# Optimization experiments

Measured on AMD Instinct MI355X. Metric: run time of the kernel, lower is better.

Reference implementation:

```python
import jax, jax.numpy as jnp
import numpy as np

H, W = 8, 64
HK, WK = 7, 11
N = H * W            # 512 tokens
C = 512              # embed_dim
HEADS = 8
HD = C // HEADS      # 64
SCALE = HD ** -0.5
B = 32


def build_local_mask():
    # Faithful port of the build() mask construction.
    m = np.ones([N, H + HK - 1, W + WK - 1], dtype=np.int32)
    for h in range(H):
        for w in range(W):
            m[h * W + w, h:h + HK, w:w + WK] = 0
    m = m[:, HK // 2:H + HK // 2, WK // 2:W + WK // 2].reshape(-1, N).astype(bool)
    mask = np.where(m, -1e30, 0.0).astype(np.float32)
    return jnp.asarray(mask.reshape(1, 1, N, N))


def setup_inputs() -> dict:
    key = jax.random.key(0)
    k1, k2, k3, k4 = jax.random.split(key, 4)
    return {
        "x": jax.random.normal(k1, (B, N, C), dtype=jnp.float32),
        "w_qkv": jax.random.normal(k2, (C, 3 * C), dtype=jnp.float32) * (C ** -0.5),
        "w_proj": jax.random.normal(k3, (C, C), dtype=jnp.float32) * (C ** -0.5),
        "b_proj": jax.random.normal(k4, (C,), dtype=jnp.float32) * 0.01,
        "mask": build_local_mask(),
    }


def reference(x, w_qkv, w_proj, b_proj, mask):
    b = x.shape[0]
    qkv = x @ w_qkv                                   # [B, N, 3C]
    qkv = qkv.reshape(b, N, 3, HEADS, HD)
    qkv = jnp.transpose(qkv, (2, 0, 3, 1, 4))          # [3, B, heads, N, hd]
    q, k, v = qkv[0], qkv[1], qkv[2]
    attn = jnp.einsum("bhnd,bhmd->bhnm", q * SCALE, k) + mask  # [B, heads, N, N]
    attn = jax.nn.softmax(attn, axis=-1)
    out = jnp.einsum("bhnm,bhmd->bhnd", attn, v)       # [B, heads, N, hd]
    out = jnp.transpose(out, (0, 2, 1, 3)).reshape(b, N, C)
    return out @ w_proj + b_proj
```

## Files before the change

### kernel.cpp

```cpp
#include <hip/hip_runtime.h>
#include <hip/hip_bf16.h>

typedef __attribute__((ext_vector_type(8))) __bf16 bf16x8;
typedef __attribute__((ext_vector_type(4))) float f32x4;

__device__ __forceinline__ unsigned short f2bf(float f) {
    unsigned int u = __float_as_uint(f);
    unsigned int r = u + 0x7FFFu + ((u >> 16) & 1u);
    return (unsigned short)(r >> 16);
}

__device__ __forceinline__ void async_copy16(const unsigned short* g, unsigned short* l) {
    __builtin_amdgcn_global_load_lds(
        (__attribute__((address_space(1))) void*)(g),
        (__attribute__((address_space(3))) void*)(l), 16, 0, 0);
}

__global__ __launch_bounds__(256) void cvt_f32_bf16(const float4* __restrict__ in,
                                                    uint4* __restrict__ out, int n8) {
    int i = blockIdx.x * blockDim.x + threadIdx.x;
    if (i >= n8) return;
    float4 a = in[2 * i], b = in[2 * i + 1];
    union { unsigned short s[8]; uint4 v; } r;
    r.s[0] = f2bf(a.x); r.s[1] = f2bf(a.y); r.s[2] = f2bf(a.z); r.s[3] = f2bf(a.w);
    r.s[4] = f2bf(b.x); r.s[5] = f2bf(b.y); r.s[6] = f2bf(b.z); r.s[7] = f2bf(b.w);
    out[i] = r.v;
}

__global__ __launch_bounds__(256) void transpose_cvt(const float* __restrict__ in,
                                                     unsigned short* __restrict__ out,
                                                     int R, int C) {
    __shared__ float tile[32][33];
    int c0 = blockIdx.x * 32, r0 = blockIdx.y * 32;
    int tx = threadIdx.x, ty = threadIdx.y;
    #pragma unroll
    for (int i = 0; i < 32; i += 8)
        tile[ty + i][tx] = in[(size_t)(r0 + ty + i) * C + c0 + tx];
    __syncthreads();
    #pragma unroll
    for (int i = 0; i < 32; i += 8)
        out[(size_t)(c0 + ty + i) * R + r0 + tx] = f2bf(tile[tx][ty + i]);
}

__device__ __forceinline__ void gemm_core_128(const unsigned short* __restrict__ A,
                                              const unsigned short* __restrict__ Bt,
                                              int K, int m0, int n0, f32x4 acc[4][4]) {
    __shared__ unsigned short As[128 * 64];
    __shared__ unsigned short Bs[128 * 64];
    const int lane = threadIdx.x & 63;
    const int wv   = threadIdx.x >> 6;
    const int wm = (wv >> 1) * 64, wn = (wv & 1) * 64;
    const int l15 = lane & 15, l16 = lane >> 4;

    f32x4 zz = {0.f, 0.f, 0.f, 0.f};
    #pragma unroll
    for (int i = 0; i < 4; ++i)
        #pragma unroll
        for (int j = 0; j < 4; ++j) acc[i][j] = zz;

    for (int k0 = 0; k0 < K; k0 += 64) {
        if (k0) __syncthreads();
        #pragma unroll
        for (int c = 0; c < 4; ++c) {
            int flat16 = c * 256 + (int)threadIdx.x;
            int r  = flat16 >> 3;
            int kk = (flat16 & 7) * 8;
            async_copy16(A  + (size_t)(m0 + r) * K + k0 + kk, As + flat16 * 8);
            async_copy16(Bt + (size_t)(n0 + r) * K + k0 + kk, Bs + flat16 * 8);
        }
        __syncthreads();
        #pragma unroll
        for (int kk = 0; kk < 64; kk += 32) {
            bf16x8 a[4], b[4];
            #pragma unroll
            for (int i = 0; i < 4; ++i)
                a[i] = *(const bf16x8*)(const void*)(As + (wm + i * 16 + l15) * 64 + kk + l16 * 8);
            #pragma unroll
            for (int i = 0; i < 4; ++i)
                b[i] = *(const bf16x8*)(const void*)(Bs + (wn + i * 16 + l15) * 64 + kk + l16 * 8);
            #pragma unroll
            for (int i = 0; i < 4; ++i)
                #pragma unroll
                for (int j = 0; j < 4; ++j)
                    acc[i][j] = __builtin_amdgcn_mfma_f32_16x16x32_bf16(a[i], b[j], acc[i][j], 0, 0, 0);
        }
    }
}

__global__ __launch_bounds__(256) void gemm_qkv(const unsigned short* __restrict__ xb,
                                                const unsigned short* __restrict__ wT,
                                                unsigned short* __restrict__ Qb,
                                                unsigned short* __restrict__ Kb,
                                                unsigned short* __restrict__ Vb) {
    f32x4 acc[4][4];
    int m0 = blockIdx.y * 128, n0 = blockIdx.x * 128;
    gemm_core_128(xb, wT, 512, m0, n0, acc);
    const int lane = threadIdx.x & 63, wv = threadIdx.x >> 6;
    const int wm = (wv >> 1) * 64, wn = (wv & 1) * 64;
    const int l15 = lane & 15, l16 = lane >> 4;
    #pragma unroll
    for (int j = 0; j < 4; ++j) {
        int col = n0 + wn + j * 16 + l15;
        int t = col >> 9;
        int within = col & 511;
        int h = within >> 6, d = within & 63;
        unsigned short* dst = (t == 0) ? Qb : (t == 1) ? Kb : Vb;
        float scl = (t == 0) ? 0.125f : 1.0f;
        #pragma unroll
        for (int i = 0; i < 4; ++i)
            #pragma unroll
            for (int e = 0; e < 4; ++e) {
                int row = m0 + wm + i * 16 + (l16 << 2) + e;
                int b = row >> 9, n = row & 511;
                dst[(((size_t)b * 8 + h) * 512 + n) * 64 + d] = f2bf(acc[i][j][e] * scl);
            }
    }
}

__global__ __launch_bounds__(256, 4) void attn_kernel(const unsigned short* __restrict__ Qb,
                                                      const unsigned short* __restrict__ Kb,
                                                      const unsigned short* __restrict__ Vb,
                                                      unsigned short* __restrict__ Ob) {
    __shared__ unsigned short Ks[64 * 72];
    __shared__ unsigned short Vt[64 * 72];
    __shared__ unsigned short Ps[4 * 32 * 72];

    const int bh = blockIdx.x >> 2;
    const int qt = blockIdx.x & 3;
    const int tid = threadIdx.x;
    const int lane = tid & 63;
    const int wv = tid >> 6;
    const int l15 = lane & 15, l16 = lane >> 4;
    const int b = bh >> 3, h = bh & 7;

    const unsigned short* Qp = Qb + (size_t)bh * 512 * 64;
    const unsigned short* Kp = Kb + (size_t)bh * 512 * 64;
    const unsigned short* Vp = Vb + (size_t)bh * 512 * 64;
    unsigned short* Pw = Ps + wv * 32 * 72;

    const int qrow0 = qt * 128 + wv * 32;
    const int qh = qrow0 >> 6;
    const int wq0 = qrow0 & 63;
    const int dead_g = wq0 ? 0 : 3;

    unsigned int wbits = 0;
    {
        int qw[2] = { wq0 + l15, wq0 + 16 + l15 };
        #pragma unroll
        for (int qf = 0; qf < 2; ++qf)
            #pragma unroll
            for (int g = 0; g < 4; ++g)
                #pragma unroll
                for (int j = 0; j < 4; ++j) {
                    int kw = g * 16 + (l16 << 2) + j;
                    int dw = qw[qf] - kw; dw = dw < 0 ? -dw : dw;
                    wbits |= (dw <= 5 ? 1u : 0u) << (qf * 16 + g * 4 + j);
                }
    }

    bf16x8 bQ[2][2];
    #pragma unroll
    for (int qf = 0; qf < 2; ++qf)
        #pragma unroll
        for (int kf = 0; kf < 2; ++kf)
            bQ[qf][kf] = *(const bf16x8*)(const void*)(Qp + (size_t)(qrow0 + qf * 16 + l15) * 64 + kf * 32 + l16 * 8);

    f32x4 o[2][4];
    f32x4 zz = {0.f, 0.f, 0.f, 0.f};
    float mrow[2] = {-INFINITY, -INFINITY}, lrow[2] = {0.f, 0.f};
    #pragma unroll
    for (int qf = 0; qf < 2; ++qf)
        #pragma unroll
        for (int df = 0; df < 4; ++df) o[qf][df] = zz;

    for (int kh = 0; kh < 8; ++kh) {
        int dlo = kh - 2 * qt;
        if (dlo < -3 || dlo > 4) continue;
        __syncthreads();
        #pragma unroll
        for (int c = 0; c < 2; ++c) {
            int flat16 = c * 256 + tid;
            int key = flat16 >> 3, dk = (flat16 & 7) * 8;
            *(uint4*)(void*)(Ks + key * 72 + dk) = *(const uint4*)(const void*)(Kp + ((size_t)(kh * 64 + key) * 64 + dk));
        }
        #pragma unroll
        for (int c = 0; c < 2; ++c) {
            int flat16 = c * 256 + tid;
            int key = flat16 & 63, d8 = flat16 >> 6;
            union { uint4 v; unsigned short s[8]; } t;
            t.v = *(const uint4*)(const void*)(Vp + ((size_t)(kh * 64 + key) * 64 + d8 * 8));
            #pragma unroll
            for (int e = 0; e < 8; ++e) Vt[(d8 * 8 + e) * 72 + key] = t.s[e];
        }
        __syncthreads();

        int adq = qh - kh; adq = adq < 0 ? -adq : adq;
        if (adq > 3) continue;

        f32x4 s[2][4];
        #pragma unroll
        for (int qf = 0; qf < 2; ++qf)
            #pragma unroll
            for (int g = 0; g < 4; ++g) s[qf][g] = zz;
        #pragma unroll
        for (int g = 0; g < 4; ++g) {
            if (g == dead_g) continue;
            bf16x8 aK0 = *(const bf16x8*)(const void*)(Ks + (g * 16 + l15) * 72 + 0  + l16 * 8);
            bf16x8 aK1 = *(const bf16x8*)(const void*)(Ks + (g * 16 + l15) * 72 + 32 + l16 * 8);
            #pragma unroll
            for (int qf = 0; qf < 2; ++qf) {
                s[qf][g] = __builtin_amdgcn_mfma_f32_16x16x32_bf16(aK0, bQ[qf][0], s[qf][g], 0, 0, 0);
                s[qf][g] = __builtin_amdgcn_mfma_f32_16x16x32_bf16(aK1, bQ[qf][1], s[qf][g], 0, 0, 0);
            }
        }

        float tmax[2] = {-1e30f, -1e30f};
        #pragma unroll
        for (int qf = 0; qf < 2; ++qf) {
            #pragma unroll
            for (int g = 0; g < 4; ++g) {
                if (g == dead_g) continue;
                #pragma unroll
                for (int j = 0; j < 4; ++j) {
                    float v = ((wbits >> (qf * 16 + g * 4 + j)) & 1u) ? s[qf][g][j] : -1e30f;
                    s[qf][g][j] = v;
                    tmax[qf] = fmaxf(tmax[qf], v);
                }
            }
            float t = tmax[qf];
            t = fmaxf(t, __shfl_xor(t, 16));
            t = fmaxf(t, __shfl_xor(t, 32));
            tmax[qf] = t;
        }

        #pragma unroll
        for (int qf = 0; qf < 2; ++qf) {
            float mnew = fmaxf(mrow[qf], tmax[qf]);
            float fs = __expf(mrow[qf] - mnew);
            mrow[qf] = mnew;
            lrow[qf] *= fs;
            #pragma unroll
            for (int j = 0; j < 4; ++j) {
                float fso = __shfl(fs, (l16 << 2) + j);
                #pragma unroll
                for (int df = 0; df < 4; ++df) o[qf][df][j] *= fso;
            }
        }

        #pragma unroll
        for (int qf = 0; qf < 2; ++qf) {
            float lsum = 0.f;
            #pragma unroll
            for (int g = 0; g < 4; ++g) {
                unsigned int lo, hi;
                if (g == dead_g) {
                    lo = 0u; hi = 0u;
                } else {
                    float e0 = __expf(s[qf][g][0] - mrow[qf]);
                    float e1 = __expf(s[qf][g][1] - mrow[qf]);
                    float e2 = __expf(s[qf][g][2] - mrow[qf]);
                    float e3 = __expf(s[qf][g][3] - mrow[qf]);
                    lsum += (e0 + e1) + (e2 + e3);
                    asm("v_cvt_pk_bf16_f32 %0, %1, %2" : "=v"(lo) : "v"(e0), "v"(e1));
                    asm("v_cvt_pk_bf16_f32 %0, %1, %2" : "=v"(hi) : "v"(e2), "v"(e3));
                }
                uint2 w; w.x = lo; w.y = hi;
                *(uint2*)(void*)(Pw + (qf * 16 + l15) * 72 + g * 16 + (l16 << 2)) = w;
            }
            float t = lsum;
            t += __shfl_xor(t, 16);
            t += __shfl_xor(t, 32);
            lrow[qf] += t;
        }
        asm volatile("" ::: "memory");

        #pragma unroll
        for (int kf = 0; kf < 2; ++kf) {
            bf16x8 aP0 = *(const bf16x8*)(const void*)(Pw + (0 * 16 + l15) * 72 + kf * 32 + l16 * 8);
            bf16x8 aP1 = *(const bf16x8*)(const void*)(Pw + (1 * 16 + l15) * 72 + kf * 32 + l16 * 8);
            #pragma unroll
            for (int df = 0; df < 4; ++df) {
                bf16x8 bV = *(const bf16x8*)(const void*)(Vt + (df * 16 + l15) * 72 + kf * 32 + l16 * 8);
                o[0][df] = __builtin_amdgcn_mfma_f32_16x16x32_bf16(aP0, bV, o[0][df], 0, 0, 0);
                o[1][df] = __builtin_amdgcn_mfma_f32_16x16x32_bf16(aP1, bV, o[1][df], 0, 0, 0);
            }
        }
    }

    #pragma unroll
    for (int qf = 0; qf < 2; ++qf) {
        float linv = 1.0f / lrow[qf];
        #pragma unroll
        for (int j = 0; j < 4; ++j) {
            float lj = __shfl(linv, (l16 << 2) + j);
            int q = qrow0 + qf * 16 + (l16 << 2) + j;
            size_t base = ((size_t)b * 512 + q) * 512 + h * 64;
            #pragma unroll
            for (int df = 0; df < 4; ++df)
                Ob[base + df * 16 + l15] = f2bf(o[qf][df][j] * lj);
        }
    }
}

__global__ __launch_bounds__(256) void gemm_proj(const unsigned short* __restrict__ Ab,
                                                 const unsigned short* __restrict__ wT,
                                                 const float* __restrict__ bias,
                                                 float* __restrict__ out) {
    f32x4 acc[4][4];
    int m0 = blockIdx.y * 128, n0 = blockIdx.x * 128;
    gemm_core_128(Ab, wT, 512, m0, n0, acc);
    const int lane = threadIdx.x & 63, wv = threadIdx.x >> 6;
    const int wm = (wv >> 1) * 64, wn = (wv & 1) * 64;
    const int l15 = lane & 15, l16 = lane >> 4;
    #pragma unroll
    for (int j = 0; j < 4; ++j) {
        int col = n0 + wn + j * 16 + l15;
        float bb = bias[col];
        #pragma unroll
        for (int i = 0; i < 4; ++i)
            #pragma unroll
            for (int e = 0; e < 4; ++e) {
                int row = m0 + wm + i * 16 + (l16 << 2) + e;
                out[(size_t)row * 512 + col] = acc[i][j][e] + bb;
            }
    }
}

extern "C" void kernel_launch(void* const* d_in, const int* in_sizes, int n_in,
                              void* d_out, int out_size, void* d_ws, size_t ws_size,
                              hipStream_t stream) {
    const float* x      = (const float*)d_in[0];
    const float* w_qkv  = (const float*)d_in[1];
    const float* w_proj = (const float*)d_in[2];
    const float* b_proj = (const float*)d_in[3];
    float* out = (float*)d_out;

    char* ws = (char*)d_ws;
    unsigned short* xb     = (unsigned short*)(ws);
    unsigned short* wqkvT  = (unsigned short*)(ws + 16777216);
    unsigned short* wprojT = (unsigned short*)(ws + 18350080);
    unsigned short* Qb     = (unsigned short*)(ws + 18874368);
    unsigned short* Kb     = (unsigned short*)(ws + 35651584);
    unsigned short* Vb     = (unsigned short*)(ws + 52428800);
    unsigned short* Ob     = xb;

    cvt_f32_bf16<<<4096, 256, 0, stream>>>((const float4*)x, (uint4*)xb, 1048576);
    transpose_cvt<<<dim3(48, 16), dim3(32, 8), 0, stream>>>(w_qkv, wqkvT, 512, 1536);
    transpose_cvt<<<dim3(16, 16), dim3(32, 8), 0, stream>>>(w_proj, wprojT, 512, 512);
    gemm_qkv<<<dim3(12, 128), 256, 0, stream>>>(xb, wqkvT, Qb, Kb, Vb);
    attn_kernel<<<1024, 256, 0, stream>>>(Qb, Kb, Vb, Ob);
    gemm_proj<<<dim3(4, 128), 256, 0, stream>>>(Ob, wprojT, b_proj, out);
}
```

Baseline: 104.3 us.

## Rewrite QKV GEMM with 256x256 tiles, double-buffered async loads, block swizzle

Replaces the 128x128 QKV projection GEMM with a 512-thread kernel that computes 256x256 output tiles. It double-buffers the A and B tiles in LDS using async global-to-LDS copies, so the next K-slice loads while MFMAs run on the current one. It also swizzles block IDs across N tiles to improve L2 reuse. The larger tiles raise arithmetic intensity and cut grid count, at the cost of 128KB of LDS per block and higher register pressure, which limits occupancy.

New measurement: 118.3 us. 1.13x slower.

```diff
diff --git a/kernel.cpp b/kernel.cpp
--- a/kernel.cpp
+++ b/kernel.cpp
@@ -87,32 +87,107 @@
     }
 }
 
-__global__ __launch_bounds__(256) void gemm_qkv(const unsigned short* __restrict__ xb,
-                                                const unsigned short* __restrict__ wT,
-                                                unsigned short* __restrict__ Qb,
-                                                unsigned short* __restrict__ Kb,
-                                                unsigned short* __restrict__ Vb) {
-    f32x4 acc[4][4];
-    int m0 = blockIdx.y * 128, n0 = blockIdx.x * 128;
-    gemm_core_128(xb, wT, 512, m0, n0, acc);
-    const int lane = threadIdx.x & 63, wv = threadIdx.x >> 6;
-    const int wm = (wv >> 1) * 64, wn = (wv & 1) * 64;
+__global__ __launch_bounds__(512, 2) void gemm_qkv256(const unsigned short* __restrict__ xb,
+                                                      const unsigned short* __restrict__ wT,
+                                                      unsigned short* __restrict__ Qb,
+                                                      unsigned short* __restrict__ Kb,
+                                                      unsigned short* __restrict__ Vb) {
+    constexpr int K  = 512;
+    constexpr int NT = K / 64;
+    __shared__ unsigned short As[2][256 * 64];
+    __shared__ unsigned short Bs[2][256 * 64];
+
+    const int tid  = threadIdx.x;
+    const int lane = tid & 63;
+    const int wv   = tid >> 6;
+    const int wr = wv >> 2, wc = wv & 3;
     const int l15 = lane & 15, l16 = lane >> 4;
+
+    const int bid = blockIdx.x;
+    const int swz = (bid & 7) * 48 + (bid >> 3);
+    const int m0 = (swz / 6) * 256;
+    const int n0 = (swz % 6) * 256;
+
+    const int r_st  = tid >> 3;
+    const int kc_st = (tid & 7) * 8;
+    const unsigned short* Arow = xb + (size_t)(m0 + r_st) * K + kc_st;
+    const unsigned short* Brow = wT + (size_t)(n0 + r_st) * K + kc_st;
+
+    f32x4 acc[8][4];
+    f32x4 zz = {0.f, 0.f, 0.f, 0.f};
+    #pragma unroll
+    for (int i = 0; i < 8; ++i)
+        #pragma unroll
+        for (int j = 0; j < 4; ++j) acc[i][j] = zz;
+
+    #pragma unroll
+    for (int c = 0; c < 4; ++c) {
+        int flat16 = c * 512 + tid;
+        async_copy16(Arow + (size_t)c * 64 * K, As[0] + flat16 * 8);
+        async_copy16(Brow + (size_t)c * 64 * K, Bs[0] + flat16 * 8);
+    }
+
+    #pragma unroll
+    for (int t = 0; t < NT; ++t) {
+        const int cur = t & 1;
+        if (t + 1 < NT) {
+            const int k0 = (t + 1) * 64;
+            #pragma unroll
+            for (int c = 0; c < 4; ++c) {
+                int flat16 = c * 512 + tid;
+                async_copy16(Arow + (size_t)c * 64 * K + k0, As[cur ^ 1] + flat16 * 8);
+                async_copy16(Brow + (size_t)c * 64 * K + k0, Bs[cur ^ 1] + flat16 * 8);
+            }
+            asm volatile("s_waitcnt vmcnt(8)" ::: "memory");
+        } else {
+            asm volatile("s_waitcnt vmcnt(0)" ::: "memory");
+        }
+        __builtin_amdgcn_sched_barrier(0);
+        __builtin_amdgcn_s_barrier();
+        __builtin_amdgcn_sched_barrier(0);
+
+        const unsigned short* Abase = As[cur] + (wr * 128 + l15) * 64 + l16 * 8;
+        const unsigned short* Bbase = Bs[cur] + (wc * 64  + l15) * 64 + l16 * 8;
+        bf16x8 b[2][4];
+        #pragma unroll
+        for (int kk = 0; kk < 2; ++kk)
+            #pragma unroll
+            for (int j = 0; j < 4; ++j)
+                b[kk][j] = *(const bf16x8*)(const void*)(Bbase + j * 16 * 64 + kk * 32);
+
+        __builtin_amdgcn_s_setprio(1);
+        #pragma unroll
+        for (int i = 0; i < 8; ++i) {
+            bf16x8 a0 = *(const bf16x8*)(const void*)(Abase + i * 16 * 64);
+            bf16x8 a1 = *(const bf16x8*)(const void*)(Abase + i * 16 * 64 + 32);
+            #pragma unroll
+            for (int j = 0; j < 4; ++j)
+                acc[i][j] = __builtin_amdgcn_mfma_f32_16x16x32_bf16(a0, b[0][j], acc[i][j], 0, 0, 0);
+            #pragma unroll
+            for (int j = 0; j < 4; ++j)
+                acc[i][j] = __builtin_amdgcn_mfma_f32_16x16x32_bf16(a1, b[1][j], acc[i][j], 0, 0, 0);
+        }
+        __builtin_amdgcn_s_setprio(0);
+        __builtin_amdgcn_sched_barrier(0);
+        __builtin_amdgcn_s_barrier();
+        __builtin_amdgcn_sched_barrier(0);
+    }
+
     #pragma unroll
     for (int j = 0; j < 4; ++j) {
-        int col = n0 + wn + j * 16 + l15;
+        int col = n0 + wc * 64 + j * 16 + l15;
         int t = col >> 9;
         int within = col & 511;
         int h = within >> 6, d = within & 63;
         unsigned short* dst = (t == 0) ? Qb : (t == 1) ? Kb : Vb;
         float scl = (t == 0) ? 0.125f : 1.0f;
         #pragma unroll
-        for (int i = 0; i < 4; ++i)
+        for (int i = 0; i < 8; ++i)
             #pragma unroll
             for (int e = 0; e < 4; ++e) {
-                int row = m0 + wm + i * 16 + (l16 << 2) + e;
-                int b = row >> 9, n = row & 511;
-                dst[(((size_t)b * 8 + h) * 512 + n) * 64 + d] = f2bf(acc[i][j][e] * scl);
+                int row = m0 + wr * 128 + i * 16 + (l16 << 2) + e;
+                int bb = row >> 9, n = row & 511;
+                dst[(((size_t)bb * 8 + h) * 512 + n) * 64 + d] = f2bf(acc[i][j][e] * scl);
             }
     }
 }
@@ -347,7 +422,7 @@
     cvt_f32_bf16<<<4096, 256, 0, stream>>>((const float4*)x, (uint4*)xb, 1048576);
     transpose_cvt<<<dim3(48, 16), dim3(32, 8), 0, stream>>>(w_qkv, wqkvT, 512, 1536);
     transpose_cvt<<<dim3(16, 16), dim3(32, 8), 0, stream>>>(w_proj, wprojT, 512, 512);
-    gemm_qkv<<<dim3(12, 128), 256, 0, stream>>>(xb, wqkvT, Qb, Kb, Vb);
+    gemm_qkv256<<<384, 512, 0, stream>>>(xb, wqkvT, Qb, Kb, Vb);
     attn_kernel<<<1024, 256, 0, stream>>>(Qb, Kb, Vb, Ob);
     gemm_proj<<<dim3(4, 128), 256, 0, stream>>>(Ob, wprojT, b_proj, out);
 }
```

## Use 256x128 QKV GEMM tiles with 8 waves and XCD-aware block mapping

Applied to the files above, without the earlier changes.

Replaces the 128x128 QKV projection GEMM with a dedicated kernel that uses 512 threads computing 256x128 output tiles, so each B tile loaded into LDS is reused across twice as many rows. Blocks are remapped so consecutive M tiles land on the same XCD, which is meant to improve L2 reuse of the activation and weight tiles. The larger tile uses more LDS per block and launches fewer blocks (768), which may reduce occupancy. The loads are still single-buffered and unpipelined.

After: 120.5 us. 15.5% more time.

```diff
diff --git a/kernel.cpp b/kernel.cpp
--- a/kernel.cpp
+++ b/kernel.cpp
@@ -87,20 +87,72 @@
     }
 }
 
-__global__ __launch_bounds__(256) void gemm_qkv(const unsigned short* __restrict__ xb,
-                                                const unsigned short* __restrict__ wT,
-                                                unsigned short* __restrict__ Qb,
-                                                unsigned short* __restrict__ Kb,
-                                                unsigned short* __restrict__ Vb) {
+__global__ __launch_bounds__(512, 2) void gemm_qkv_bm(const unsigned short* __restrict__ xb,
+                                                      const unsigned short* __restrict__ wT,
+                                                      unsigned short* __restrict__ Qb,
+                                                      unsigned short* __restrict__ Kb,
+                                                      unsigned short* __restrict__ Vb) {
+    constexpr int K = 512;
+    __shared__ unsigned short As[256 * 64];
+    __shared__ unsigned short Bs[128 * 64];
+
+    const int tid  = threadIdx.x;
+    const int lane = tid & 63;
+    const int wv   = tid >> 6;
+    const int wr = wv >> 1, wc = wv & 1;
+    const int l15 = lane & 15, l16 = lane >> 4;
+
+    const int bid = blockIdx.x;
+    const int xcd = bid & 7, idx = bid >> 3;
+    const int mt  = xcd * 8 + idx / 12;
+    const int nt  = idx % 12;
+    const int m0 = mt * 256, n0 = nt * 128;
+
     f32x4 acc[4][4];
-    int m0 = blockIdx.y * 128, n0 = blockIdx.x * 128;
-    gemm_core_128(xb, wT, 512, m0, n0, acc);
-    const int lane = threadIdx.x & 63, wv = threadIdx.x >> 6;
-    const int wm = (wv >> 1) * 64, wn = (wv & 1) * 64;
-    const int l15 = lane & 15, l16 = lane >> 4;
+    f32x4 zz = {0.f, 0.f, 0.f, 0.f};
+    #pragma unroll
+    for (int i = 0; i < 4; ++i)
+        #pragma unroll
+        for (int j = 0; j < 4; ++j) acc[i][j] = zz;
+
+    const int r_st  = tid >> 3;
+    const int kk_st = (tid & 7) * 8;
+    const unsigned short* Arow = xb + (size_t)(m0 + r_st) * K + kk_st;
+    const unsigned short* Brow = wT + (size_t)(n0 + r_st) * K + kk_st;
+
+    for (int k0 = 0; k0 < K; k0 += 64) {
+        if (k0) __syncthreads();
+        #pragma unroll
+        for (int c = 0; c < 4; ++c) {
+            int flat16 = c * 512 + tid;
+            async_copy16(Arow + (size_t)c * 64 * K + k0, As + flat16 * 8);
+        }
+        #pragma unroll
+        for (int c = 0; c < 2; ++c) {
+            int flat16 = c * 512 + tid;
+            async_copy16(Brow + (size_t)c * 64 * K + k0, Bs + flat16 * 8);
+        }
+        __syncthreads();
+        #pragma unroll
+        for (int kk = 0; kk < 64; kk += 32) {
+            bf16x8 a[4], b[4];
+            #pragma unroll
+            for (int i = 0; i < 4; ++i)
+                a[i] = *(const bf16x8*)(const void*)(As + (wr * 64 + i * 16 + l15) * 64 + kk + l16 * 8);
+            #pragma unroll
+            for (int j = 0; j < 4; ++j)
+                b[j] = *(const bf16x8*)(const void*)(Bs + (wc * 64 + j * 16 + l15) * 64 + kk + l16 * 8);
+            #pragma unroll
+            for (int i = 0; i < 4; ++i)
+                #pragma unroll
+                for (int j = 0; j < 4; ++j)
+                    acc[i][j] = __builtin_amdgcn_mfma_f32_16x16x32_bf16(a[i], b[j], acc[i][j], 0, 0, 0);
+        }
+    }
+
     #pragma unroll
     for (int j = 0; j < 4; ++j) {
-        int col = n0 + wn + j * 16 + l15;
+        int col = n0 + wc * 64 + j * 16 + l15;
         int t = col >> 9;
         int within = col & 511;
         int h = within >> 6, d = within & 63;
@@ -110,9 +162,9 @@
         for (int i = 0; i < 4; ++i)
             #pragma unroll
             for (int e = 0; e < 4; ++e) {
-                int row = m0 + wm + i * 16 + (l16 << 2) + e;
-                int b = row >> 9, n = row & 511;
-                dst[(((size_t)b * 8 + h) * 512 + n) * 64 + d] = f2bf(acc[i][j][e] * scl);
+                int row = m0 + wr * 64 + i * 16 + (l16 << 2) + e;
+                int bb = row >> 9, n = row & 511;
+                dst[(((size_t)bb * 8 + h) * 512 + n) * 64 + d] = f2bf(acc[i][j][e] * scl);
             }
     }
 }
@@ -347,7 +399,7 @@
     cvt_f32_bf16<<<4096, 256, 0, stream>>>((const float4*)x, (uint4*)xb, 1048576);
     transpose_cvt<<<dim3(48, 16), dim3(32, 8), 0, stream>>>(w_qkv, wqkvT, 512, 1536);
     transpose_cvt<<<dim3(16, 16), dim3(32, 8), 0, stream>>>(w_proj, wprojT, 512, 512);
-    gemm_qkv<<<dim3(12, 128), 256, 0, stream>>>(xb, wqkvT, Qb, Kb, Vb);
+    gemm_qkv_bm<<<768, 512, 0, stream>>>(xb, wqkvT, Qb, Kb, Vb);
     attn_kernel<<<1024, 256, 0, stream>>>(Qb, Kb, Vb, Ob);
     gemm_proj<<<dim3(4, 128), 256, 0, stream>>>(Ob, wprojT, b_proj, out);
 }
```
